# Optimization experiments

Hardware: AMD Instinct MI355X
Metric: run time of the kernel (lower is better)

## Reference

```python
import jax, jax.numpy as jnp
import numpy as np

L = 2          # num_hidden_layers
B, S, H = 2, 2048, 1024
NH, DH = 16, 64   # heads, head dim
FF = 4096
EPS = 1e-5


def setup_inputs() -> dict:
    key = jax.random.key(0)
    ks = jax.random.split(key, 20)
    s = 0.02
    inp = {
        "hidden_states": jax.random.normal(ks[0], (B, S, H), jnp.float32),
        "attention_mask": jnp.zeros((B, 1, 1, S), jnp.float32),
        "Wq": jax.random.normal(ks[1], (L, H, H), jnp.float32) * s,
        "bq": jnp.zeros((L, H), jnp.float32),
        "Wk": jax.random.normal(ks[2], (L, H, H), jnp.float32) * s,
        "bk": jnp.zeros((L, H), jnp.float32),
        "Wv": jax.random.normal(ks[3], (L, H, H), jnp.float32) * s,
        "bv": jnp.zeros((L, H), jnp.float32),
        "Wao": jax.random.normal(ks[4], (L, H, H), jnp.float32) * s,
        "bao": jnp.zeros((L, H), jnp.float32),
        "ln1_g": jnp.ones((L, H), jnp.float32),
        "ln1_b": jnp.zeros((L, H), jnp.float32),
        "Wi": jax.random.normal(ks[5], (L, H, FF), jnp.float32) * s,
        "bi": jnp.zeros((L, FF), jnp.float32),
        "Wo": jax.random.normal(ks[6], (L, FF, H), jnp.float32) * s,
        "bo": jnp.zeros((L, H), jnp.float32),
        "ln2_g": jnp.ones((L, H), jnp.float32),
        "ln2_b": jnp.zeros((L, H), jnp.float32),
    }
    return inp


def _layernorm(x, g, b):
    m = jnp.mean(x, axis=-1, keepdims=True)
    v = jnp.var(x, axis=-1, keepdims=True)
    return (x - m) * jax.lax.rsqrt(v + EPS) * g + b


def _split_heads(x):
    # [B,S,H] -> [B,NH,S,DH]
    return x.reshape(B, S, NH, DH).transpose(0, 2, 1, 3)


def _layer(x, mask, Wq, bq, Wk, bk, Wv, bv, Wao, bao, g1, b1, Wi, bi, Wo, bo, g2, b2):
    q = _split_heads(x @ Wq + bq)
    k = _split_heads(x @ Wk + bk)
    v = _split_heads(x @ Wv + bv)
    scores = jnp.einsum('bhqd,bhkd->bhqk', q, k) / np.sqrt(DH).astype(np.float32)
    scores = scores + mask  # additive attention mask
    probs = jax.nn.softmax(scores, axis=-1)
    ctx = jnp.einsum('bhqk,bhkd->bhqd', probs, v)
    ctx = ctx.transpose(0, 2, 1, 3).reshape(B, S, H)
    x = _layernorm(ctx @ Wao + bao + x, g1, b1)
    ffn = jax.nn.gelu(x @ Wi + bi, approximate=False) @ Wo + bo
    return _layernorm(ffn + x, g2, b2)


def reference(hidden_states, attention_mask, Wq, bq, Wk, bk, Wv, bv, Wao, bao,
              ln1_g, ln1_b, Wi, bi, Wo, bo, ln2_g, ln2_b):
    x = hidden_states
    for i in range(L):
        x = _layer(x, attention_mask,
                   Wq[i], bq[i], Wk[i], bk[i], Wv[i], bv[i], Wao[i], bao[i],
                   ln1_g[i], ln1_b[i], Wi[i], bi[i], Wo[i], bo[i], ln2_g[i], ln2_b[i])
    return x
```

## Files before the change

### kernel.cpp

```cpp
#include <hip/hip_runtime.h>

typedef _Float16 half_t;
typedef _Float16 half8  __attribute__((ext_vector_type(8)));
typedef _Float16 half4v __attribute__((ext_vector_type(4)));
typedef float    f32x4  __attribute__((ext_vector_type(4)));

#define AS1 __attribute__((address_space(1)))
#define AS3 __attribute__((address_space(3)))

#define MODE_H16  0
#define MODE_F32R 1
#define MODE_GELU 2

__device__ __forceinline__ f32x4 zero4() {
    f32x4 z; z[0] = 0.f; z[1] = 0.f; z[2] = 0.f; z[3] = 0.f; return z;
}

__device__ __forceinline__ half8 lds_frag(const half_t* p) {
    union { uint4 u; half8 h; } c;
    c.u = *(const uint4*)p;
    return c.h;
}

__device__ __forceinline__ float gelu_f(float v) {
    float t = v * v;
    float u = v * (1.595769122f + 0.0713548163f * t);
    return v / (1.f + __expf(-u));
}

__device__ __forceinline__ void gl_lds16(const half_t* g, half_t* l) {
    __builtin_amdgcn_global_load_lds(
        (AS1 unsigned int*)(unsigned long long)(const void*)g,
        (AS3 unsigned int*)l,
        16, 0, 0);
}



__device__ __forceinline__ void stage_half(
    const half_t* __restrict__ G, half_t* L, int K, int srow, int sck, int w)
{
    gl_lds16(G + (size_t)srow * K + sck,        L + w * 512);
    gl_lds16(G + (size_t)(64 + srow) * K + sck, L + 4096 + w * 512);
}

#define LDA(MH)                                                              \
    _Pragma("unroll")                                                        \
    for (int m = 0; m < 4; m++) {                                            \
        af[m][0] = lds_frag(&Ad[abase + (MH) * 4096 + m * 1024 + c0]);       \
        af[m][1] = lds_frag(&Ad[abase + (MH) * 4096 + m * 1024 + c1]);       \
    }

#define LDB(NH)                                                              \
    _Pragma("unroll")                                                        \
    for (int n = 0; n < 2; n++) {                                            \
        bf[NH][n][0] = lds_frag(&Bd[bbase + (NH) * 2048 + n * 1024 + c0]);   \
        bf[NH][n][1] = lds_frag(&Bd[bbase + (NH) * 2048 + n * 1024 + c1]);   \
    }

#define MFMA_Q(MH, NH)                                                       \
    _Pragma("unroll")                                                        \
    for (int m = 0; m < 4; m++)                                              \
        _Pragma("unroll")                                                    \
        for (int n = 0; n < 2; n++) {                                        \
            acc[(MH)*4 + m][(NH)*2 + n] =                                    \
                __builtin_amdgcn_mfma_f32_16x16x32_f16(                      \
                    af[m][0], bf[NH][n][0], acc[(MH)*4 + m][(NH)*2 + n],     \
                    0, 0, 0);                                                \
            acc[(MH)*4 + m][(NH)*2 + n] =                                    \
                __builtin_amdgcn_mfma_f32_16x16x32_f16(                      \
                    af[m][1], bf[NH][n][1], acc[(MH)*4 + m][(NH)*2 + n],     \
                    0, 0, 0);                                                \
        }

__device__ __forceinline__ void mfma_core256(
    const half_t* __restrict__ Ag, const half_t* __restrict__ Bg, int K,
    half_t* As, half_t* Bs, f32x4 (&acc)[8][4])
{
    const int tid  = threadIdx.x;
    const int w    = tid >> 6, lane = tid & 63;
    const int wm   = w >> 2, wn = w & 3;
    const int g    = lane >> 4, ml = lane & 15, m7 = ml & 7;
    const int srow = tid >> 3;
    const int sck  = ((tid & 7) ^ (srow & 7)) * 8;

#pragma unroll
    for (int i = 0; i < 8; i++)
#pragma unroll
        for (int j = 0; j < 4; j++) acc[i][j] = zero4();

    const int abase = (wm * 128 + ml) * 64;
    const int bbase = (wn * 64 + ml) * 64;
    const int c0 = (g ^ m7) * 8, c1 = ((4 + g) ^ m7) * 8;

    stage_half(Ag, As, K, srow, sck, w);
    stage_half(Ag + (size_t)128 * K, As + 8192, K, srow, sck, w);
    stage_half(Bg, Bs, K, srow, sck, w);
    stage_half(Bg + (size_t)128 * K, Bs + 8192, K, srow, sck, w);
    asm volatile("s_waitcnt vmcnt(0)" ::: "memory");
    __builtin_amdgcn_s_barrier();

    const int NT = K >> 6;
    half8 af[4][2];
    half8 bf[2][2][2];

    for (int t = 0; t < NT; ++t) {
        half_t* Ad = As + (t & 1) * 16384;
        half_t* Bd = Bs + (t & 1) * 16384;
        half_t* An = As + ((t + 1) & 1) * 16384;
        half_t* Bn = Bs + ((t + 1) & 1) * 16384;
        const half_t* Agn = Ag + (t + 1) * 64;
        const half_t* Bgn = Bg + (t + 1) * 64;
        const bool pf = (t + 1 < NT);

        LDA(0)
        LDB(0)
        if (pf) {
            stage_half(Agn, An, K, srow, sck, w);
            stage_half(Agn + (size_t)128 * K, An + 8192, K, srow, sck, w);
        }
        __builtin_amdgcn_s_barrier();
        __builtin_amdgcn_s_setprio(1);
        MFMA_Q(0, 0)
        __builtin_amdgcn_s_setprio(0);
        __builtin_amdgcn_s_barrier();

        LDB(1)
        if (pf) {
            stage_half(Bgn, Bn, K, srow, sck, w);
            stage_half(Bgn + (size_t)128 * K, Bn + 8192, K, srow, sck, w);
        }
        __builtin_amdgcn_s_barrier();
        __builtin_amdgcn_s_setprio(1);
        MFMA_Q(0, 1)
        __builtin_amdgcn_s_setprio(0);
        __builtin_amdgcn_s_barrier();

        LDA(1)
        __builtin_amdgcn_s_barrier();
        __builtin_amdgcn_s_setprio(1);
        MFMA_Q(1, 1)
        __builtin_amdgcn_s_setprio(0);
        __builtin_amdgcn_s_barrier();

        __builtin_amdgcn_s_setprio(1);
        MFMA_Q(1, 0)
        __builtin_amdgcn_s_setprio(0);
        asm volatile("s_waitcnt vmcnt(0)" ::: "memory");
        __builtin_amdgcn_s_barrier();
    }
}

__global__ __launch_bounds__(512, 2) void gemm256_bt(
    const half_t* __restrict__ A,
    const half_t* __restrict__ Bt,
    const float*  __restrict__ bias,
    const float*  __restrict__ res,
    void* __restrict__ out,
    int M, int N, int K, int mode)
{
    __shared__ __align__(16) half_t As[2 * 16384];
    __shared__ __align__(16) half_t Bs[2 * 16384];

    const int m0 = blockIdx.y * 256, n0 = blockIdx.x * 256;
    f32x4 acc[8][4];
    mfma_core256(A + (size_t)m0 * K, Bt + (size_t)n0 * K, K, As, Bs, acc);

    const int tid = threadIdx.x;
    const int w   = tid >> 6, lane = tid & 63;
    const int wm  = w >> 2, wn = w & 3;
    const int g   = lane >> 4, ml = lane & 15;
    const int gm0 = m0 + wm * 128, gn0 = n0 + wn * 64;

#pragma unroll
    for (int nj = 0; nj < 4; nj++) {
        int col = gn0 + nj * 16 + ml;
        float bv = bias[col];
#pragma unroll
        for (int mi = 0; mi < 8; mi++) {
#pragma unroll
            for (int r = 0; r < 4; r++) {
                int row = gm0 + mi * 16 + g * 4 + r;
                float v = acc[mi][nj][r] + bv;
                size_t idx = (size_t)row * N + col;
                if (mode == MODE_F32R) {
                    ((float*)out)[idx] = v + res[idx];
                } else if (mode == MODE_GELU) {
                    ((half_t*)out)[idx] = (half_t)gelu_f(v);
                } else {
                    ((half_t*)out)[idx] = (half_t)v;
                }
            }
        }
    }
}

__global__ __launch_bounds__(512, 2) void gemm256_qkv(
    const half_t* __restrict__ A,
    const half_t* __restrict__ Bt,
    const float*  __restrict__ bq,
    const float*  __restrict__ bk,
    const float*  __restrict__ bv,
    half_t* __restrict__ Qo, half_t* __restrict__ Ko, half_t* __restrict__ Vto,
    int M, int K)
{
    __shared__ __align__(16) half_t As[2 * 16384];
    __shared__ __align__(16) half_t Bs[2 * 16384];

    const int m0 = blockIdx.y * 256, n0 = blockIdx.x * 256;
    f32x4 acc[8][4];
    mfma_core256(A + (size_t)m0 * K, Bt + (size_t)n0 * K, K, As, Bs, acc);

    const int tid = threadIdx.x;
    const int w   = tid >> 6, lane = tid & 63;
    const int wm  = w >> 2, wn = w & 3;
    const int g   = lane >> 4, ml = lane & 15;

    const int seg   = n0 >> 10;
    const int nbase = (n0 & 1023) + wn * 64;
    const float* bias = (seg == 0) ? bq : (seg == 1) ? bk : bv;
    const int gm0 = m0 + wm * 128;

    if (seg < 2) {
        half_t* O = (seg == 0) ? Qo : Ko;
#pragma unroll
        for (int nj = 0; nj < 4; nj++) {
            int col = nbase + nj * 16 + ml;
            float bvv = bias[col];
#pragma unroll
            for (int mi = 0; mi < 8; mi++)
#pragma unroll
                for (int r = 0; r < 4; r++)
                    O[(size_t)(gm0 + mi * 16 + g * 4 + r) * 1024 + col] =
                        (half_t)(acc[mi][nj][r] + bvv);
        }
    } else {
#pragma unroll
        for (int nj = 0; nj < 4; nj++) {
            int col = nbase + nj * 16 + ml;
            float bvv = bias[col];
#pragma unroll
            for (int mi = 0; mi < 8; mi++) {
                int rowb = gm0 + mi * 16 + g * 4;
                int bb = rowb >> 11, sl = rowb & 2047;
                half4v v4;
#pragma unroll
                for (int r = 0; r < 4; r++) v4[r] = (half_t)(acc[mi][nj][r] + bvv);
                *(half4v*)&Vto[((size_t)bb * 1024 + col) * 2048 + sl] = v4;
            }
        }
    }
}

__global__ __launch_bounds__(256) void gemm_bt64(
    const half_t* __restrict__ A,
    const half_t* __restrict__ Bt,
    const float*  __restrict__ bias,
    const float*  __restrict__ res,
    float* __restrict__ out,
    int M, int N, int K)
{
    __shared__ __align__(16) half_t As[128 * 64];
    __shared__ __align__(16) half_t Bs[64 * 64];

    const int tid  = threadIdx.x;
    const int w    = tid >> 6, lane = tid & 63;
    const int m0   = blockIdx.y * 128, n0 = blockIdx.x * 64;
    const int g    = lane >> 4, ml = lane & 15, m7 = ml & 7;
    const int mo   = w * 32;
    const int r8   = lane >> 3;
    const int sck  = ((lane & 7) ^ (r8 & 7)) * 8;

    f32x4 acc[2][4];
#pragma unroll
    for (int i = 0; i < 2; i++)
#pragma unroll
        for (int j = 0; j < 4; j++) acc[i][j] = zero4();

    const half_t* Ag = A  + (size_t)m0 * K;
    const half_t* Bg = Bt + (size_t)n0 * K;

    for (int k0 = 0; k0 < K; k0 += 64) {
        __syncthreads();
#pragma unroll
        for (int i = 0; i < 4; i++) {
            int t = w * 4 + i;
            gl_lds16(Ag + (size_t)(t * 8 + r8) * K + k0 + sck, &As[t * 512]);
        }
#pragma unroll
        for (int i = 0; i < 2; i++) {
            int t = w * 2 + i;
            gl_lds16(Bg + (size_t)(t * 8 + r8) * K + k0 + sck, &Bs[t * 512]);
        }
        __syncthreads();
#pragma unroll
        for (int kk = 0; kk < 2; kk++) {
            const int co = ((kk * 4 + g) ^ m7) * 8;
            half8 af[2], bf[4];
#pragma unroll
            for (int i = 0; i < 2; i++) af[i] = lds_frag(&As[(mo + i * 16 + ml) * 64 + co]);
#pragma unroll
            for (int j = 0; j < 4; j++) bf[j] = lds_frag(&Bs[(j * 16 + ml) * 64 + co]);
#pragma unroll
            for (int i = 0; i < 2; i++)
#pragma unroll
                for (int j = 0; j < 4; j++)
                    acc[i][j] = __builtin_amdgcn_mfma_f32_16x16x32_f16(af[i], bf[j], acc[i][j], 0, 0, 0);
        }
    }

    const int gm0 = m0 + mo;
#pragma unroll
    for (int j = 0; j < 4; j++) {
        int col = n0 + j * 16 + ml;
        float bv = bias[col];
#pragma unroll
        for (int i = 0; i < 2; i++) {
#pragma unroll
            for (int r = 0; r < 4; r++) {
                int row = gm0 + i * 16 + g * 4 + r;
                size_t idx = (size_t)row * N + col;
                out[idx] = acc[i][j][r] + bv + res[idx];
            }
        }
    }
}

__global__ __launch_bounds__(256, 4) void flash_attn(
    const half_t* __restrict__ Q,
    const half_t* __restrict__ Kq,
    const half_t* __restrict__ Vt,
    const float*  __restrict__ mask,
    half_t* __restrict__ opart,
    float2* __restrict__ mlpart,
    int S, int H)
{
    __shared__ __align__(16) half_t Ks[64 * 64];
    __shared__ __align__(16) half_t Vs[64 * 64];
    __shared__ __align__(16) half_t Ps[4 * 32 * 64];

    const int qt = blockIdx.x, h = blockIdx.y, z = blockIdx.z;
    const int b = z >> 1, hf = z & 1;
    const int tid = threadIdx.x, w = tid >> 6, lane = tid & 63;
    const int g = lane >> 4, ml = lane & 15, m7 = ml & 7;
    const int NHloc = gridDim.y;
    const int BNHS = 2 * NHloc * S;

    const int q0 = qt * 128 + w * 32;
    const half_t* Qg = Q  + ((size_t)(b * S + q0)) * H + h * 64;
    const half_t* Kg = Kq + ((size_t)b * S) * H + h * 64;
    const half_t* Vg = Vt + ((size_t)b * H + h * 64) * (size_t)S;
    const float*  mk = mask + (size_t)b * S;

    half8 qf[2][2];
#pragma unroll
    for (int qi = 0; qi < 2; qi++)
#pragma unroll
        for (int kk = 0; kk < 2; kk++)
            qf[qi][kk] = *(const half8*)(Qg + (size_t)(qi * 16 + ml) * H + kk * 32 + g * 8);

    float m_[2] = {-1e30f, -1e30f}, l_[2] = {0.f, 0.f};
    f32x4 o[2][4];
#pragma unroll
    for (int qi = 0; qi < 2; qi++)
#pragma unroll
        for (int df = 0; df < 4; df++) o[qi][df] = zero4();

    half_t* Pw = &Ps[w * 32 * 64];
    const int srow = tid >> 3;
    const int sc   = tid & 7;

    const int kvbeg = hf * (S >> 1), kvend = kvbeg + (S >> 1);
    for (int kv0 = kvbeg; kv0 < kvend; kv0 += 64) {
        __syncthreads();
#pragma unroll
        for (int t = 0; t < 2; t++) {
            int row = t * 32 + srow;
            int ck  = sc ^ (row & 7);
            gl_lds16(Kg + (size_t)(kv0 + row) * H + ck * 8, &Ks[(t * 256 + w * 64) * 8]);
            gl_lds16(Vg + (size_t)row * S + kv0 + ck * 8,   &Vs[(t * 256 + w * 64) * 8]);
        }
        __syncthreads();

        f32x4 s[2][4];
#pragma unroll
        for (int kvf = 0; kvf < 4; kvf++) {
            half8 k0 = lds_frag(&Ks[(kvf * 16 + ml) * 64 + ((0 + g) ^ m7) * 8]);
            half8 k1 = lds_frag(&Ks[(kvf * 16 + ml) * 64 + ((4 + g) ^ m7) * 8]);
            s[0][kvf] = __builtin_amdgcn_mfma_f32_16x16x32_f16(k0, qf[0][0], zero4(), 0, 0, 0);
            s[0][kvf] = __builtin_amdgcn_mfma_f32_16x16x32_f16(k1, qf[0][1], s[0][kvf], 0, 0, 0);
            s[1][kvf] = __builtin_amdgcn_mfma_f32_16x16x32_f16(k0, qf[1][0], zero4(), 0, 0, 0);
            s[1][kvf] = __builtin_amdgcn_mfma_f32_16x16x32_f16(k1, qf[1][1], s[1][kvf], 0, 0, 0);
        }
#pragma unroll
        for (int kvf = 0; kvf < 4; kvf++) {
            float4 mv = *(const float4*)(mk + kv0 + kvf * 16 + g * 4);
#pragma unroll
            for (int qi = 0; qi < 2; qi++) {
                s[qi][kvf][0] = s[qi][kvf][0] * 0.125f + mv.x;
                s[qi][kvf][1] = s[qi][kvf][1] * 0.125f + mv.y;
                s[qi][kvf][2] = s[qi][kvf][2] * 0.125f + mv.z;
                s[qi][kvf][3] = s[qi][kvf][3] * 0.125f + mv.w;
            }
        }
        float alpha[2];
#pragma unroll
        for (int qi = 0; qi < 2; qi++) {
            float mx = -1e30f;
#pragma unroll
            for (int kvf = 0; kvf < 4; kvf++)
#pragma unroll
                for (int r = 0; r < 4; r++) mx = fmaxf(mx, s[qi][kvf][r]);
            mx = fmaxf(mx, __shfl_xor(mx, 16));
            mx = fmaxf(mx, __shfl_xor(mx, 32));
            float mnew = fmaxf(m_[qi], mx);
            alpha[qi]  = __expf(m_[qi] - mnew);
            m_[qi] = mnew;
            float ps = 0.f;
#pragma unroll
            for (int kvf = 0; kvf < 4; kvf++)
#pragma unroll
                for (int r = 0; r < 4; r++) {
                    float pv = __expf(s[qi][kvf][r] - mnew);
                    s[qi][kvf][r] = pv; ps += pv;
                }
            ps += __shfl_xor(ps, 16);
            ps += __shfl_xor(ps, 32);
            l_[qi] = l_[qi] * alpha[qi] + ps;
#pragma unroll
            for (int kvf = 0; kvf < 4; kvf++) {
                half4v pk;
#pragma unroll
                for (int r = 0; r < 4; r++) pk[r] = (half_t)s[qi][kvf][r];
                *(half4v*)(Pw + (qi * 16 + ml) * 64 +
                           (((kvf * 2 + (g >> 1)) ^ m7) * 8) + (g & 1) * 4) = pk;
            }
        }
#pragma unroll
        for (int qi = 0; qi < 2; qi++) {
#pragma unroll
            for (int r = 0; r < 4; r++) {
                float a = __shfl(alpha[qi], (lane & 48) + g * 4 + r);
#pragma unroll
                for (int df = 0; df < 4; df++) o[qi][df][r] *= a;
            }
        }
#pragma unroll
        for (int kk = 0; kk < 2; kk++) {
            half8 pa0 = lds_frag(&Pw[(ml)      * 64 + ((kk * 4 + g) ^ m7) * 8]);
            half8 pa1 = lds_frag(&Pw[(16 + ml) * 64 + ((kk * 4 + g) ^ m7) * 8]);
#pragma unroll
            for (int df = 0; df < 4; df++) {
                half8 vb = lds_frag(&Vs[(df * 16 + ml) * 64 + ((kk * 4 + g) ^ m7) * 8]);
                o[0][df] = __builtin_amdgcn_mfma_f32_16x16x32_f16(pa0, vb, o[0][df], 0, 0, 0);
                o[1][df] = __builtin_amdgcn_mfma_f32_16x16x32_f16(pa1, vb, o[1][df], 0, 0, 0);
            }
        }
    }

    const size_t rowbase = (size_t)hf * BNHS + ((size_t)(b * NHloc + h)) * S + q0;
#pragma unroll
    for (int qi = 0; qi < 2; qi++) {
#pragma unroll
        for (int r = 0; r < 4; r++) {
            size_t ro = (rowbase + qi * 16 + g * 4 + r) * 64;
#pragma unroll
            for (int df = 0; df < 4; df++)
                opart[ro + df * 16 + ml] = (half_t)o[qi][df][r];
        }
    }
    if (g == 0) {
#pragma unroll
        for (int qi = 0; qi < 2; qi++)
            mlpart[rowbase + qi * 16 + ml] = make_float2(m_[qi], l_[qi]);
    }
}

__global__ __launch_bounds__(256) void flash_merge(
    const half_t* __restrict__ opart,
    const float2* __restrict__ mlpart,
    half_t* __restrict__ ctx)
{
    int gid = blockIdx.x * 256 + threadIdx.x;
    int row = gid >> 4, dg = (gid & 15) * 4;
    float2 a = mlpart[row], c = mlpart[65536 + row];
    float m  = fmaxf(a.x, c.x);
    float w1 = __expf(a.x - m), w2 = __expf(c.x - m);
    float inv = 1.f / (w1 * a.y + w2 * c.y);
    half4v o1 = *(const half4v*)&opart[(size_t)row * 64 + dg];
    half4v o2 = *(const half4v*)&opart[(size_t)(65536 + row) * 64 + dg];
    int b = row >> 15, hq = row & 32767;
    int h = hq >> 11, q = hq & 2047;
    half4v o;
#pragma unroll
    for (int i = 0; i < 4; i++)
        o[i] = (half_t)((w1 * (float)o1[i] + w2 * (float)o2[i]) * inv);
    *(half4v*)&ctx[((size_t)(b * 2048 + q)) * 1024 + h * 64 + dg] = o;
}

__global__ __launch_bounds__(256) void transpose_cast(
    const float* __restrict__ W, half_t* __restrict__ Wt, int Kd, int Nd)
{
    __shared__ float tile[32][33];
    size_t zoff = (size_t)blockIdx.z * Kd * Nd;
    const float* Wz = W + zoff;
    half_t* Wtz = Wt + zoff;
    int n0 = blockIdx.x * 32, k0 = blockIdx.y * 32;
    int tx = threadIdx.x & 31, ty = threadIdx.x >> 5;
#pragma unroll
    for (int j = 0; j < 4; j++)
        tile[ty + j * 8][tx] = Wz[(size_t)(k0 + ty + j * 8) * Nd + n0 + tx];
    __syncthreads();
#pragma unroll
    for (int j = 0; j < 4; j++)
        Wtz[(size_t)(n0 + ty + j * 8) * Kd + k0 + tx] = (half_t)tile[tx][ty + j * 8];
}

__global__ __launch_bounds__(256) void transpose_qkv(
    const float* __restrict__ Wq, const float* __restrict__ Wk,
    const float* __restrict__ Wv, half_t* __restrict__ WT)
{
    __shared__ float tile[32][33];
    int z = blockIdx.z, l = z / 3, which = z % 3;
    const float* W = ((which == 0) ? Wq : (which == 1) ? Wk : Wv) + (size_t)l * 1024 * 1024;
    half_t* D = WT + ((size_t)l * 3 + which) * 1024 * 1024;
    int n0 = blockIdx.x * 32, k0 = blockIdx.y * 32;
    int tx = threadIdx.x & 31, ty = threadIdx.x >> 5;
#pragma unroll
    for (int j = 0; j < 4; j++)
        tile[ty + j * 8][tx] = W[(size_t)(k0 + ty + j * 8) * 1024 + n0 + tx];
    __syncthreads();
#pragma unroll
    for (int j = 0; j < 4; j++)
        D[(size_t)(n0 + ty + j * 8) * 1024 + k0 + tx] = (half_t)tile[tx][ty + j * 8];
}

__global__ __launch_bounds__(256) void cast_f32_f16(
    const float* __restrict__ in, half_t* __restrict__ out)
{
    int i = blockIdx.x * 256 + threadIdx.x;
    float4 v = ((const float4*)in)[i];
    half4v o; o[0] = (half_t)v.x; o[1] = (half_t)v.y; o[2] = (half_t)v.z; o[3] = (half_t)v.w;
    *(half4v*)(out + (size_t)i * 4) = o;
}

__global__ __launch_bounds__(256) void layernorm_k(
    const float* __restrict__ in,
    const float* __restrict__ gam, const float* __restrict__ bet,
    float* __restrict__ outf, half_t* __restrict__ outh)
{
    int row = blockIdx.x, tid = threadIdx.x;
    const float4 v = ((const float4*)(in + (size_t)row * 1024))[tid];
    float s = v.x + v.y + v.z + v.w;
    float q = v.x * v.x + v.y * v.y + v.z * v.z + v.w * v.w;
    for (int off = 32; off; off >>= 1) { s += __shfl_down(s, off); q += __shfl_down(q, off); }
    __shared__ float ss[4], sq[4];
    int w = tid >> 6;
    if ((tid & 63) == 0) { ss[w] = s; sq[w] = q; }
    __syncthreads();
    float S_ = ss[0] + ss[1] + ss[2] + ss[3];
    float Q_ = sq[0] + sq[1] + sq[2] + sq[3];
    float mean = S_ * (1.f / 1024.f);
    float var  = Q_ * (1.f / 1024.f) - mean * mean;
    float rstd = rsqrtf(var + 1e-5f);
    float4 gm = ((const float4*)gam)[tid];
    float4 bt = ((const float4*)bet)[tid];
    float y0 = (v.x - mean) * rstd * gm.x + bt.x;
    float y1 = (v.y - mean) * rstd * gm.y + bt.y;
    float y2 = (v.z - mean) * rstd * gm.z + bt.z;
    float y3 = (v.w - mean) * rstd * gm.w + bt.w;
    ((float4*)(outf + (size_t)row * 1024))[tid] = make_float4(y0, y1, y2, y3);
    half4v oh; oh[0] = (half_t)y0; oh[1] = (half_t)y1; oh[2] = (half_t)y2; oh[3] = (half_t)y3;
    *(half4v*)(outh + (size_t)row * 1024 + tid * 4) = oh;
}

extern "C" void kernel_launch(void* const* d_in, const int* in_sizes, int n_in,
                              void* d_out, int out_size, void* d_ws, size_t ws_size,
                              hipStream_t stream)
{
    const int Lc = 2, Bb = 2, S = 2048, Hh = 1024, NH = 16, FF = 4096;
    const int M = Bb * S;

    const float* hs   = (const float*)d_in[0];
    const float* mask = (const float*)d_in[1];
    const float* Wq   = (const float*)d_in[2];  const float* bq  = (const float*)d_in[3];
    const float* Wk   = (const float*)d_in[4];  const float* bk  = (const float*)d_in[5];
    const float* Wv   = (const float*)d_in[6];  const float* bv  = (const float*)d_in[7];
    const float* Wao  = (const float*)d_in[8];  const float* bao = (const float*)d_in[9];
    const float* g1   = (const float*)d_in[10]; const float* b1  = (const float*)d_in[11];
    const float* Wi   = (const float*)d_in[12]; const float* bi  = (const float*)d_in[13];
    const float* Wo   = (const float*)d_in[14]; const float* bo  = (const float*)d_in[15];
    const float* g2   = (const float*)d_in[16]; const float* b2  = (const float*)d_in[17];

    char* p = (char*)d_ws;
    auto take = [&](size_t bytes) { char* r = p; p += (bytes + 255) & ~(size_t)255; return r; };

    half_t* WqkvT = (half_t*)take((size_t)Lc * 3 * Hh * Hh * 2);
    half_t* WaoT  = (half_t*)take((size_t)Lc * Hh * Hh * 2);
    half_t* WiT   = (half_t*)take((size_t)Lc * Hh * FF * 2);
    half_t* WoT   = (half_t*)take((size_t)Lc * FF * Hh * 2);
    half_t* xb    = (half_t*)take((size_t)M * Hh * 2);
    half_t* Qb    = (half_t*)take((size_t)M * Hh * 2);
    half_t* Kb2   = (half_t*)take((size_t)M * Hh * 2);
    half_t* Vtb   = (half_t*)take((size_t)M * Hh * 2);
    (void)          take((size_t)M * Hh * 2);
    half_t* h1    = Qb;
    float*  t0    = (float*)take((size_t)M * Hh * 4);
    float*  x1f   = (float*)take((size_t)M * Hh * 4);
    half_t* x1b   = (half_t*)take((size_t)M * Hh * 2);

    half_t* opart  = (half_t*)t0;
    float2* mlpart = (float2*)x1b;

    dim3 tb(256);

    transpose_qkv<<<dim3(32, 32, Lc * 3), tb, 0, stream>>>(Wq, Wk, Wv, WqkvT);
    transpose_cast<<<dim3(32, 32, Lc), tb, 0, stream>>>(Wao, WaoT, Hh, Hh);
    transpose_cast<<<dim3(FF / 32, 32, Lc), tb, 0, stream>>>(Wi, WiT, Hh, FF);
    transpose_cast<<<dim3(32, FF / 32, Lc), tb, 0, stream>>>(Wo, WoT, FF, Hh);
    cast_f32_f16<<<dim3(M * Hh / 1024), tb, 0, stream>>>(hs, xb);

    const float* xres = hs;
    for (int l = 0; l < Lc; l++) {
        const half_t* WqkvTl = WqkvT + (size_t)l * 3 * Hh * Hh;
        const half_t* WaoTl  = WaoT  + (size_t)l * Hh * Hh;
        const half_t* WiTl   = WiT   + (size_t)l * Hh * FF;
        const half_t* WoTl   = WoT   + (size_t)l * FF * Hh;

        gemm256_qkv<<<dim3(3072 / 256, M / 256), dim3(512), 0, stream>>>(
            xb, WqkvTl, bq + l * Hh, bk + l * Hh, bv + l * Hh, Qb, Kb2, Vtb, M, Hh);

        flash_attn<<<dim3(S / 128, NH, Bb * 2), tb, 0, stream>>>(
            Qb, Kb2, Vtb, mask, opart, mlpart, S, Hh);
        flash_merge<<<dim3(Bb * NH * S * 16 / 256), tb, 0, stream>>>(opart, mlpart, xb);

        gemm_bt64<<<dim3(Hh / 64, M / 128), tb, 0, stream>>>(
            xb, WaoTl, bao + l * Hh, xres, t0, M, Hh, Hh);
        layernorm_k<<<dim3(M), tb, 0, stream>>>(t0, g1 + l * Hh, b1 + l * Hh, x1f, x1b);

        gemm256_bt<<<dim3(FF / 256, M / 256), dim3(512), 0, stream>>>(
            x1b, WiTl, bi + l * FF, nullptr, h1, M, FF, Hh, MODE_GELU);
        gemm_bt64<<<dim3(Hh / 64, M / 128), tb, 0, stream>>>(
            h1, WoTl, bo + l * Hh, x1f, t0, M, Hh, FF);

        float* outf = (l == Lc - 1) ? (float*)d_out : x1f;
        layernorm_k<<<dim3(M), tb, 0, stream>>>(t0, g2 + l * Hh, b2 + l * Hh, outf, xb);
        xres = x1f;
    }
}
```

Baseline: 683.4 us.

## Split attention KV into four chunks with register prefetch and exp2 softmax

Flash attention now splits the KV range into four partitions instead of two and uses a flattened 1D grid. K/V tiles are prefetched into registers and written to LDS after compute, replacing the direct global-to-LDS loads. The softmax switches to exp2 with log2e folded into the scale, skips rescaling when the row max grows by less than a threshold, and raises wave priority around the MFMA sections. The merge kernel combines four partials from a dedicated workspace, which adds extra partial-result traffic and a larger buffer in exchange for more parallel blocks.

Result: slower. 809.9 us (+18.5%).

```diff
diff --git a/kernel.cpp b/kernel.cpp
--- a/kernel.cpp
+++ b/kernel.cpp
@@ -26,6 +26,10 @@
     float t = v * v;
     float u = v * (1.595769122f + 0.0713548163f * t);
     return v / (1.f + __expf(-u));
+}
+
+__device__ __forceinline__ float fexp2(float x) {
+    return __builtin_amdgcn_exp2f(x);
 }
 
 __device__ __forceinline__ void gl_lds16(const half_t* g, half_t* l) {
@@ -74,7 +78,8 @@
         }
 
 __device__ __forceinline__ void mfma_core256(
-    const half_t* __restrict__ Ag, const half_t* __restrict__ Bg, int K,
+    const half_t* __restrict__ Ag, const half_t* __restrict__ Bg,
+    int K, int KT,
     half_t* As, half_t* Bs, f32x4 (&acc)[8][4])
 {
     const int tid  = threadIdx.x;
@@ -100,18 +105,17 @@
     asm volatile("s_waitcnt vmcnt(0)" ::: "memory");
     __builtin_amdgcn_s_barrier();
 
-    const int NT = K >> 6;
     half8 af[4][2];
     half8 bf[2][2][2];
 
-    for (int t = 0; t < NT; ++t) {
+    for (int t = 0; t < KT; ++t) {
         half_t* Ad = As + (t & 1) * 16384;
         half_t* Bd = Bs + (t & 1) * 16384;
         half_t* An = As + ((t + 1) & 1) * 16384;
         half_t* Bn = Bs + ((t + 1) & 1) * 16384;
         const half_t* Agn = Ag + (t + 1) * 64;
         const half_t* Bgn = Bg + (t + 1) * 64;
-        const bool pf = (t + 1 < NT);
+        const bool pf = (t + 1 < KT);
 
         LDA(0)
         LDB(0)
@@ -164,7 +168,7 @@
 
     const int m0 = blockIdx.y * 256, n0 = blockIdx.x * 256;
     f32x4 acc[8][4];
-    mfma_core256(A + (size_t)m0 * K, Bt + (size_t)n0 * K, K, As, Bs, acc);
+    mfma_core256(A + (size_t)m0 * K, Bt + (size_t)n0 * K, K, K >> 6, As, Bs, acc);
 
     const int tid = threadIdx.x;
     const int w   = tid >> 6, lane = tid & 63;
@@ -209,7 +213,7 @@
 
     const int m0 = blockIdx.y * 256, n0 = blockIdx.x * 256;
     f32x4 acc[8][4];
-    mfma_core256(A + (size_t)m0 * K, Bt + (size_t)n0 * K, K, As, Bs, acc);
+    mfma_core256(A + (size_t)m0 * K, Bt + (size_t)n0 * K, K, K >> 6, As, Bs, acc);
 
     const int tid = threadIdx.x;
     const int w   = tid >> 6, lane = tid & 63;
@@ -339,12 +343,19 @@
     __shared__ __align__(16) half_t Vs[64 * 64];
     __shared__ __align__(16) half_t Ps[4 * 32 * 64];
 
-    const int qt = blockIdx.x, h = blockIdx.y, z = blockIdx.z;
-    const int b = z >> 1, hf = z & 1;
+    const float LOG2E = 1.44269504f;
+    const float SCL2  = 0.125f * 1.44269504f;
+
+    const int f  = blockIdx.x;
+    const int z  = f & 7;
+    const int j  = f >> 3;
+    const int h  = j >> 4;
+    const int qt = j & 15;
+    const int b = z >> 2, hf = z & 3;
+
     const int tid = threadIdx.x, w = tid >> 6, lane = tid & 63;
     const int g = lane >> 4, ml = lane & 15, m7 = ml & 7;
-    const int NHloc = gridDim.y;
-    const int BNHS = 2 * NHloc * S;
+    const int BNHS = 2 * 16 * S;
 
     const int q0 = qt * 128 + w * 32;
     const half_t* Qg = Q  + ((size_t)(b * S + q0)) * H + h * 64;
@@ -370,19 +381,45 @@
     const int srow = tid >> 3;
     const int sc   = tid & 7;
 
-    const int kvbeg = hf * (S >> 1), kvend = kvbeg + (S >> 1);
-    for (int kv0 = kvbeg; kv0 < kvend; kv0 += 64) {
-        __syncthreads();
+    uint4 kr[2], vr[2];
+
+    const int kvbeg = hf * (S >> 2);
+    const int NT = (S >> 2) >> 6;
+
+    auto load_regs = [&](int kv0) {
 #pragma unroll
         for (int t = 0; t < 2; t++) {
             int row = t * 32 + srow;
             int ck  = sc ^ (row & 7);
-            gl_lds16(Kg + (size_t)(kv0 + row) * H + ck * 8, &Ks[(t * 256 + w * 64) * 8]);
-            gl_lds16(Vg + (size_t)row * S + kv0 + ck * 8,   &Vs[(t * 256 + w * 64) * 8]);
-        }
-        __syncthreads();
+            kr[t] = *(const uint4*)(Kg + (size_t)(kv0 + row) * H + ck * 8);
+            vr[t] = *(const uint4*)(Vg + (size_t)row * S + kv0 + ck * 8);
+        }
+    };
+    auto write_lds = [&]() {
+#pragma unroll
+        for (int t = 0; t < 2; t++) {
+            int row = t * 32 + srow;
+            *(uint4*)&Ks[row * 64 + sc * 8] = kr[t];
+            *(uint4*)&Vs[row * 64 + sc * 8] = vr[t];
+        }
+    };
+
+    load_regs(kvbeg);
+    write_lds();
+    __syncthreads();
+
+    for (int it = 0; it < NT; ++it) {
+        const int kv0 = kvbeg + it * 64;
+        const bool pf = (it + 1 < NT);
+
+        float4 mvv[4];
+#pragma unroll
+        for (int kvf = 0; kvf < 4; kvf++)
+            mvv[kvf] = *(const float4*)(mk + kv0 + kvf * 16 + g * 4);
+        if (pf) load_regs(kv0 + 64);
 
         f32x4 s[2][4];
+        __builtin_amdgcn_s_setprio(1);
 #pragma unroll
         for (int kvf = 0; kvf < 4; kvf++) {
             half8 k0 = lds_frag(&Ks[(kvf * 16 + ml) * 64 + ((0 + g) ^ m7) * 8]);
@@ -392,18 +429,23 @@
             s[1][kvf] = __builtin_amdgcn_mfma_f32_16x16x32_f16(k0, qf[1][0], zero4(), 0, 0, 0);
             s[1][kvf] = __builtin_amdgcn_mfma_f32_16x16x32_f16(k1, qf[1][1], s[1][kvf], 0, 0, 0);
         }
+        __builtin_amdgcn_s_setprio(0);
+
 #pragma unroll
         for (int kvf = 0; kvf < 4; kvf++) {
-            float4 mv = *(const float4*)(mk + kv0 + kvf * 16 + g * 4);
+            float mv0 = mvv[kvf].x * LOG2E, mv1 = mvv[kvf].y * LOG2E;
+            float mv2 = mvv[kvf].z * LOG2E, mv3 = mvv[kvf].w * LOG2E;
 #pragma unroll
             for (int qi = 0; qi < 2; qi++) {
-                s[qi][kvf][0] = s[qi][kvf][0] * 0.125f + mv.x;
-                s[qi][kvf][1] = s[qi][kvf][1] * 0.125f + mv.y;
-                s[qi][kvf][2] = s[qi][kvf][2] * 0.125f + mv.z;
-                s[qi][kvf][3] = s[qi][kvf][3] * 0.125f + mv.w;
+                s[qi][kvf][0] = s[qi][kvf][0] * SCL2 + mv0;
+                s[qi][kvf][1] = s[qi][kvf][1] * SCL2 + mv1;
+                s[qi][kvf][2] = s[qi][kvf][2] * SCL2 + mv2;
+                s[qi][kvf][3] = s[qi][kvf][3] * SCL2 + mv3;
             }
         }
+
         float alpha[2];
+        bool  defer[2];
 #pragma unroll
         for (int qi = 0; qi < 2; qi++) {
             float mx = -1e30f;
@@ -413,20 +455,23 @@
                 for (int r = 0; r < 4; r++) mx = fmaxf(mx, s[qi][kvf][r]);
             mx = fmaxf(mx, __shfl_xor(mx, 16));
             mx = fmaxf(mx, __shfl_xor(mx, 32));
-            float mnew = fmaxf(m_[qi], mx);
-            alpha[qi]  = __expf(m_[qi] - mnew);
+            defer[qi] = __all(mx <= m_[qi] + 11.5f);
+            float mnew, al;
+            if (defer[qi]) { mnew = m_[qi]; al = 1.f; }
+            else           { mnew = fmaxf(m_[qi], mx); al = fexp2(m_[qi] - mnew); }
+            alpha[qi] = al;
             m_[qi] = mnew;
             float ps = 0.f;
 #pragma unroll
             for (int kvf = 0; kvf < 4; kvf++)
 #pragma unroll
                 for (int r = 0; r < 4; r++) {
-                    float pv = __expf(s[qi][kvf][r] - mnew);
+                    float pv = fexp2(s[qi][kvf][r] - mnew);
                     s[qi][kvf][r] = pv; ps += pv;
                 }
             ps += __shfl_xor(ps, 16);
             ps += __shfl_xor(ps, 32);
-            l_[qi] = l_[qi] * alpha[qi] + ps;
+            l_[qi] = l_[qi] * al + ps;
 #pragma unroll
             for (int kvf = 0; kvf < 4; kvf++) {
                 half4v pk;
@@ -438,13 +483,17 @@
         }
 #pragma unroll
         for (int qi = 0; qi < 2; qi++) {
-#pragma unroll
-            for (int r = 0; r < 4; r++) {
-                float a = __shfl(alpha[qi], (lane & 48) + g * 4 + r);
-#pragma unroll
-                for (int df = 0; df < 4; df++) o[qi][df][r] *= a;
+            if (!defer[qi]) {
+#pragma unroll
+                for (int r = 0; r < 4; r++) {
+                    float a = __shfl(alpha[qi], (lane & 48) + g * 4 + r);
+#pragma unroll
+                    for (int df = 0; df < 4; df++) o[qi][df][r] *= a;
+                }
             }
         }
+
+        __builtin_amdgcn_s_setprio(1);
 #pragma unroll
         for (int kk = 0; kk < 2; kk++) {
             half8 pa0 = lds_frag(&Pw[(ml)      * 64 + ((kk * 4 + g) ^ m7) * 8]);
@@ -456,9 +505,16 @@
                 o[1][df] = __builtin_amdgcn_mfma_f32_16x16x32_f16(pa1, vb, o[1][df], 0, 0, 0);
             }
         }
-    }
-
-    const size_t rowbase = (size_t)hf * BNHS + ((size_t)(b * NHloc + h)) * S + q0;
+        __builtin_amdgcn_s_setprio(0);
+
+        __syncthreads();
+        if (pf) {
+            write_lds();
+            __syncthreads();
+        }
+    }
+
+    const size_t rowbase = (size_t)hf * BNHS + ((size_t)(b * 16 + h)) * S + q0;
 #pragma unroll
     for (int qi = 0; qi < 2; qi++) {
 #pragma unroll
@@ -483,18 +539,25 @@
 {
     int gid = blockIdx.x * 256 + threadIdx.x;
     int row = gid >> 4, dg = (gid & 15) * 4;
-    float2 a = mlpart[row], c = mlpart[65536 + row];
-    float m  = fmaxf(a.x, c.x);
-    float w1 = __expf(a.x - m), w2 = __expf(c.x - m);
-    float inv = 1.f / (w1 * a.y + w2 * c.y);
-    half4v o1 = *(const half4v*)&opart[(size_t)row * 64 + dg];
-    half4v o2 = *(const half4v*)&opart[(size_t)(65536 + row) * 64 + dg];
+    float2 a0 = mlpart[row];
+    float2 a1 = mlpart[65536 + row];
+    float2 a2 = mlpart[131072 + row];
+    float2 a3 = mlpart[196608 + row];
+    float m = fmaxf(fmaxf(a0.x, a1.x), fmaxf(a2.x, a3.x));
+    float w0 = fexp2(a0.x - m), w1 = fexp2(a1.x - m);
+    float w2 = fexp2(a2.x - m), w3 = fexp2(a3.x - m);
+    float inv = 1.f / (w0 * a0.y + w1 * a1.y + w2 * a2.y + w3 * a3.y);
+    half4v o0 = *(const half4v*)&opart[(size_t)row * 64 + dg];
+    half4v o1 = *(const half4v*)&opart[((size_t)65536 + row) * 64 + dg];
+    half4v o2 = *(const half4v*)&opart[((size_t)131072 + row) * 64 + dg];
+    half4v o3 = *(const half4v*)&opart[((size_t)196608 + row) * 64 + dg];
     int b = row >> 15, hq = row & 32767;
     int h = hq >> 11, q = hq & 2047;
     half4v o;
 #pragma unroll
     for (int i = 0; i < 4; i++)
-        o[i] = (half_t)((w1 * (float)o1[i] + w2 * (float)o2[i]) * inv);
+        o[i] = (half_t)((w0 * (float)o0[i] + w1 * (float)o1[i] +
+                         w2 * (float)o2[i] + w3 * (float)o3[i]) * inv);
     *(half4v*)&ctx[((size_t)(b * 2048 + q)) * 1024 + h * 64 + dg] = o;
 }
 
@@ -608,9 +671,10 @@
     float*  t0    = (float*)take((size_t)M * Hh * 4);
     float*  x1f   = (float*)take((size_t)M * Hh * 4);
     half_t* x1b   = (half_t*)take((size_t)M * Hh * 2);
-
-    half_t* opart  = (half_t*)t0;
-    float2* mlpart = (float2*)x1b;
+    char*   fpart = take((size_t)36 * 1024 * 1024);
+
+    half_t* opart  = (half_t*)fpart;
+    float2* mlpart = (float2*)(fpart + (size_t)4 * 65536 * 64 * 2);
 
     dim3 tb(256);
 
@@ -630,7 +694,7 @@
         gemm256_qkv<<<dim3(3072 / 256, M / 256), dim3(512), 0, stream>>>(
             xb, WqkvTl, bq + l * Hh, bk + l * Hh, bv + l * Hh, Qb, Kb2, Vtb, M, Hh);
 
-        flash_attn<<<dim3(S / 128, NH, Bb * 2), tb, 0, stream>>>(
+        flash_attn<<<dim3(2048), tb, 0, stream>>>(
             Qb, Kb2, Vtb, mask, opart, mlpart, S, Hh);
         flash_merge<<<dim3(Bb * NH * S * 16 / 256), tb, 0, stream>>>(opart, mlpart, xb);
 
```
